# Kernel tuning notes

Measured on AMD Instinct MI355X. Metric: run time of the kernel, lower is better.

Reference implementation:

```python
import jax, jax.numpy as jnp
import numpy as np

B, T, L = 256, 512, 64


def setup_inputs() -> dict:
    key = jax.random.key(0)
    k1, k2, k3 = jax.random.split(key, 3)
    labels = jax.random.randint(k1, (B, T), 0, L)
    y_true = jax.nn.one_hot(labels, L, dtype=jnp.float32)  # [B,T,L] one-hot gold path
    y_pred = jax.random.normal(k2, (B, T, L), dtype=jnp.float32)  # emission scores
    # glorot_uniform init for trans [L,L]
    limit = np.sqrt(6.0 / (L + L)).astype(np.float32)
    trans = jax.random.uniform(k3, (L, L), dtype=jnp.float32, minval=-limit, maxval=limit)
    return {"y_true": y_true, "y_pred": y_pred, "trans": trans}


def reference(y_true, y_pred, trans):
    # ignore_last_label=False -> mask is None, all labels used.
    # Forward-algorithm log-partition via scan over time.
    init = y_pred[:, 0]  # [B,L]

    def step(state, emit_t):
        # state: [B,L] log-alpha; emit_t: [B,L]
        new = jax.nn.logsumexp(state[:, :, None] + trans[None, :, :], axis=1) + emit_t
        return new, None

    emits = jnp.swapaxes(y_pred[:, 1:], 0, 1)  # [T-1,B,L]
    last, _ = jax.lax.scan(step, init, emits)
    log_norm = jax.nn.logsumexp(last, axis=1, keepdims=True)  # [B,1]

    # path_score: per-label emission score + transition score along gold path
    point_score = jnp.sum(y_pred * y_true, axis=(1, 2))[:, None]  # [B,1]
    trans_score = jnp.einsum('bti,btj,ij->b', y_true[:, :-1], y_true[:, 1:], trans)[:, None]
    return -(point_score + trans_score - log_norm)  # [B,1] loss per example
```

## Files before the change

### kernel.cpp

```cpp
#include <hip/hip_runtime.h>
#include <hip/hip_bf16.h>
#include <cstdint>
#include <cstddef>


constexpr int Bc = 256, Tc = 512, Lc = 64;
#define LOG64F 4.1588830833596715f
#define WS_SCAL_OFF (16u << 20)

typedef __attribute__((ext_vector_type(8))) short v8s;
typedef __attribute__((ext_vector_type(4))) float v4f;
typedef __attribute__((ext_vector_type(4))) unsigned int v4u;
typedef __attribute__((ext_vector_type(2))) unsigned int v2u;

__device__ __forceinline__ float lane_bcast(float v, int lane) {
    return __uint_as_float(__builtin_amdgcn_readlane(__float_as_uint(v), lane));
}
__device__ __forceinline__ int lane_bcast_i(int v, int lane) {
    return __builtin_amdgcn_readlane(v, lane);
}
__device__ __forceinline__ unsigned pk2(float x, float y) {
    __hip_bfloat162 h = __float22bfloat162_rn(make_float2(x, y));
    unsigned r; __builtin_memcpy(&r, &h, 4); return r;
}
__device__ __forceinline__ v8s as_v8s(v4u u) {
    v8s r; __builtin_memcpy(&r, &u, 16); return r;
}

__global__ __launch_bounds__(256, 2) void crf_pass1(
    const float* __restrict__ y_true,
    const float* __restrict__ y_pred,
    const float* __restrict__ trans,
    unsigned short* __restrict__ wsm,
    float* __restrict__ wss)
{
    const int tid = threadIdx.x, lane = tid & 63, wv = tid >> 6;
    const int w = blockIdx.x * 4 + wv;
    const int batch = w >> 3, chunk = w & 7;
    const int q = lane >> 4, m16 = lane & 15;
    const int rsub = q, csub = m16;

    __shared__ float strans[Lc * Lc];
    __shared__ alignas(16) float fbuf[4][2][4][Lc];

    {
        const v4f* t4 = (const v4f*)trans;
        #pragma unroll
        for (int k = 0; k < 4; ++k) {
            v4f v = t4[k * 256 + tid];
            *(v4f*)&strans[(k * 256 + tid) * 4] = v;
        }
    }
    __syncthreads();

    v8s Af[4][2];
    #pragma unroll
    for (int I = 0; I < 4; ++I) {
        #pragma unroll
        for (int K = 0; K < 2; ++K) {
            float e[8];
            #pragma unroll
            for (int jj = 0; jj < 8; ++jj) {
                const int sig = (jj & 3) + 4 * q + 16 * (jj >> 2) + 32 * K;
                e[jj] = __expf(strans[sig * Lc + 16 * I + m16]);
            }
            v4u u;
            u.x = pk2(e[0], e[1]); u.y = pk2(e[2], e[3]);
            u.z = pk2(e[4], e[5]); u.w = pk2(e[6], e[7]);
            Af[I][K] = as_v8s(u);
        }
    }

    const float* yp = y_pred + (size_t)batch * Tc * Lc;
    const float* yt = y_true + (size_t)batch * Tc * Lc;
    const v4f* yp4 = (const v4f*)yp;
    const v4f* yt4 = (const v4f*)yt;

    const int base = chunk * 64;
    int lbl_carry;
    {
        const float bt = yt[base * Lc + lane];
        lbl_carry = (int)__builtin_ctzll(__ballot(bt > 0.5f));
    }
    float psum = 0.0f, tsum = 0.0f, c = 0.0f;

    auto ld4 = [&](const v4f* p, int baseRow) -> v4f {
        int r = baseRow + rsub; r = (r < Tc - 1) ? r : (Tc - 1);
        return p[r * 16 + csub];
    };

    const int r0 = base + 1;
    v4f cyp = ld4(yp4, r0),     cyt = ld4(yt4, r0);
    v4f nyp = ld4(yp4, r0 + 4), nyt = ld4(yt4, r0 + 4);
    v4f myp = ld4(yp4, r0 + 8), myt = ld4(yt4, r0 + 8);

    {
        const float k0 = lane_bcast(cyp.x, 0)  + LOG64F;
        const float k1 = lane_bcast(cyp.x, 16) + LOG64F;
        const float k2 = lane_bcast(cyp.x, 32) + LOG64F;
        const float k3 = lane_bcast(cyp.x, 48) + LOG64F;
        c += ((k0 + k1) + (k2 + k3));
        const float kk = (rsub & 1) ? ((rsub & 2) ? k3 : k1)
                                    : ((rsub & 2) ? k2 : k0);
        v4f f;
        f.x = __expf(cyp.x - kk); f.y = __expf(cyp.y - kk);
        f.z = __expf(cyp.z - kk); f.w = __expf(cyp.w - kk);
        *(v4f*)&fbuf[wv][0][rsub][4 * csub] = f;
    }

    v8s Bfr[2][4];
    #pragma unroll
    for (int K = 0; K < 2; ++K) {
        #pragma unroll
        for (int J = 0; J < 4; ++J) {
            v8s bb;
            #pragma unroll
            for (int jj = 0; jj < 8; ++jj) {
                const bool one = (csub == 4 * q + (jj & 3)) && (J == (jj >> 2) + 2 * K);
                bb[jj] = one ? (short)0x3F80 : (short)0;
            }
            Bfr[K][J] = bb;
        }
    }

    const v4f z4 = {0.f, 0.f, 0.f, 0.f};
    v4f P[4][4];
    #pragma unroll
    for (int I = 0; I < 4; ++I) {
        #pragma unroll
        for (int J = 0; J < 4; ++J) P[I][J] = z4;
    }
    int par = 0;

    auto mstep = [&](int s) {
        v4f F[4];
        #pragma unroll
        for (int I = 0; I < 4; ++I)
            F[I] = *(const v4f*)&fbuf[wv][par][s][16 * I + 4 * q];
        #pragma unroll
        for (int I = 0; I < 4; ++I) {
            #pragma unroll
            for (int J = 0; J < 4; ++J) {
                v4f a = __builtin_amdgcn_mfma_f32_16x16x32_bf16(Af[I][0], Bfr[0][J], z4, 0, 0, 0);
                a = __builtin_amdgcn_mfma_f32_16x16x32_bf16(Af[I][1], Bfr[1][J], a, 0, 0, 0);
                P[I][J] = a * F[I];
            }
        }
        #pragma unroll
        for (int K = 0; K < 2; ++K) {
            #pragma unroll
            for (int J = 0; J < 4; ++J) {
                v4u u;
                u.x = pk2(P[2 * K][J].x,     P[2 * K][J].y);
                u.y = pk2(P[2 * K][J].z,     P[2 * K][J].w);
                u.z = pk2(P[2 * K + 1][J].x, P[2 * K + 1][J].y);
                u.w = pk2(P[2 * K + 1][J].z, P[2 * K + 1][J].w);
                Bfr[K][J] = as_v8s(u);
            }
        }
    };

    auto scores4 = [&]() {
        psum = fmaf(cyp.x, cyt.x, psum); psum = fmaf(cyp.y, cyt.y, psum);
        psum = fmaf(cyp.z, cyt.z, psum); psum = fmaf(cyp.w, cyt.w, psum);
        const float has = fmaxf(fmaxf(cyt.x, cyt.y), fmaxf(cyt.z, cyt.w));
        int lidx = 0;
        lidx = (cyt.y > 0.5f) ? 1 : lidx;
        lidx = (cyt.z > 0.5f) ? 2 : lidx;
        lidx = (cyt.w > 0.5f) ? 3 : lidx;
        const unsigned long long m = __ballot(has > 0.5f);
        const int ln0 = (int)__builtin_ctz((unsigned)(m & 0xFFFFull));
        const int ln1 = (int)__builtin_ctz((unsigned)((m >> 16) & 0xFFFFull));
        const int ln2 = (int)__builtin_ctz((unsigned)((m >> 32) & 0xFFFFull));
        const int ln3 = (int)__builtin_ctz((unsigned)(m >> 48));
        const int lbl0 = 4 * ln0 + lane_bcast_i(lidx, ln0);
        const int lbl1 = 4 * ln1 + lane_bcast_i(lidx, 16 + ln1);
        const int lbl2 = 4 * ln2 + lane_bcast_i(lidx, 32 + ln2);
        const int lbl3 = 4 * ln3 + lane_bcast_i(lidx, 48 + ln3);
        const int lpA = (rsub & 2) ? lbl1 : lbl_carry;
        const int lpB = (rsub & 2) ? lbl2 : lbl0;
        const int lp  = (rsub & 1) ? lpB : lpA;
        lbl_carry = lbl3;
        const v4f tr = *(const v4f*)&strans[lp * Lc + 4 * csub];
        tsum = fmaf(cyt.x, tr.x, tsum); tsum = fmaf(cyt.y, tr.y, tsum);
        tsum = fmaf(cyt.z, tr.z, tsum); tsum = fmaf(cyt.w, tr.w, tsum);
    };

    #pragma unroll 1
    for (int bi = 0; bi < 15; ++bi) {
        const int rb = r0 + 4 * bi;
        const v4f lyp = ld4(yp4, rb + 12), lyt = ld4(yt4, rb + 12);
        scores4();
        mstep(0); mstep(1); mstep(2); mstep(3);
        {
            const float sc = lane_bcast(P[0][0].x, 0);
            const float inv_s = 1.0f / sc;
            c += __logf(sc);
            const float k0 = lane_bcast(nyp.x, 0)  + LOG64F;
            const float k1 = lane_bcast(nyp.x, 16) + LOG64F;
            const float k2 = lane_bcast(nyp.x, 32) + LOG64F;
            const float k3 = lane_bcast(nyp.x, 48) + LOG64F;
            c += ((k0 + k1) + k2);
            if (rb + 7 <= Tc - 1) c += k3;
            const float kk = (rsub & 1) ? ((rsub & 2) ? k3 : k1)
                                        : ((rsub & 2) ? k2 : k0);
            const float sc0 = (rsub == 0) ? inv_s : 1.0f;
            v4f f;
            f.x = __expf(nyp.x - kk) * sc0; f.y = __expf(nyp.y - kk) * sc0;
            f.z = __expf(nyp.z - kk) * sc0; f.w = __expf(nyp.w - kk) * sc0;
            *(v4f*)&fbuf[wv][par ^ 1][rsub][4 * csub] = f;
        }
        par ^= 1;
        cyp = nyp; cyt = nyt; nyp = myp; nyt = myt; myp = lyp; myt = lyt;
    }

    if (chunk < 7) {
        scores4();
        mstep(0); mstep(1); mstep(2); mstep(3);
    } else {
        {
            float pd = cyp.x * cyt.x;
            pd = fmaf(cyp.y, cyt.y, pd); pd = fmaf(cyp.z, cyt.z, pd); pd = fmaf(cyp.w, cyt.w, pd);
            const float has = fmaxf(fmaxf(cyt.x, cyt.y), fmaxf(cyt.z, cyt.w));
            int lidx = 0;
            lidx = (cyt.y > 0.5f) ? 1 : lidx;
            lidx = (cyt.z > 0.5f) ? 2 : lidx;
            lidx = (cyt.w > 0.5f) ? 3 : lidx;
            const unsigned long long m = __ballot(has > 0.5f);
            const int ln0 = (int)__builtin_ctz((unsigned)(m & 0xFFFFull));
            const int ln1 = (int)__builtin_ctz((unsigned)((m >> 16) & 0xFFFFull));
            const int lbl0 = 4 * ln0 + lane_bcast_i(lidx, ln0);
            const int lbl1 = 4 * ln1 + lane_bcast_i(lidx, 16 + ln1);
            const int lpA = (rsub & 2) ? lbl1 : lbl_carry;
            const int lp  = (rsub & 1) ? lbl0 : lpA;
            const v4f tr = *(const v4f*)&strans[lp * Lc + 4 * csub];
            float td = cyt.x * tr.x;
            td = fmaf(cyt.y, tr.y, td); td = fmaf(cyt.z, tr.z, td); td = fmaf(cyt.w, tr.w, td);
            if (rsub < 3) { psum += pd; tsum += td; }
        }
        mstep(0); mstep(1); mstep(2);
    }

    unsigned short* hout = wsm + (size_t)(batch * 8 + chunk) * 4096;
    #pragma unroll
    for (int I = 0; I < 4; ++I) {
        #pragma unroll
        for (int J = 0; J < 4; ++J) {
            v2u u2;
            u2.x = pk2(P[I][J].x, P[I][J].y);
            u2.y = pk2(P[I][J].z, P[I][J].w);
            *(v2u*)(hout + (16 * J + csub) * 64 + 16 * I + 4 * q) = u2;
        }
    }
    #pragma unroll
    for (int k = 1; k < 64; k <<= 1) psum += __shfl_xor(psum, k);
    #pragma unroll
    for (int k = 1; k < 64; k <<= 1) tsum += __shfl_xor(tsum, k);
    if (lane == 0) {
        float* s = wss + (batch * 8 + chunk) * 4;
        s[0] = c; s[1] = psum; s[2] = tsum;
    }
}

__global__ __launch_bounds__(256, 1) void crf_pass2(
    const float* __restrict__ y_true,
    const float* __restrict__ y_pred,
    const unsigned short* __restrict__ wsm,
    const float* __restrict__ wss,
    float* __restrict__ out)
{
    const int tid = threadIdx.x, lane = tid & 63, wv = tid >> 6;
    const int b = blockIdx.x * 4 + wv;
    const int q = lane >> 4, m16 = lane & 15;

    __shared__ unsigned short hmat[4][4096];
    __shared__ float arow[4][Lc];

    const float* yp = y_pred + (size_t)b * Tc * Lc;
    const float* yt = y_true + (size_t)b * Tc * Lc;
    const float yp0 = yp[lane], yt0 = yt[lane];
    float psum = yp0 * yt0, tsum = 0.0f;
    float c = lane_bcast(yp0, 0);
    arow[wv][lane] = __expf(yp0 - c);

    v8s Bfr[2];
    #pragma unroll
    for (int cc = 0; cc < 2; ++cc) {
        const v4f lo = *(const v4f*)&arow[wv][32 * cc + 4 * q];
        const v4f hi = *(const v4f*)&arow[wv][32 * cc + 16 + 4 * q];
        v4u u;
        u.x = pk2(lo.x, lo.y); u.y = pk2(lo.z, lo.w);
        u.z = pk2(hi.x, hi.y); u.w = pk2(hi.z, hi.w);
        Bfr[cc] = as_v8s(u);
    }

    const v4f z4 = {0.f, 0.f, 0.f, 0.f};
    v4f P0 = z4, P1 = z4, P2 = z4, P3 = z4;

    #pragma unroll 1
    for (int kk = 0; kk < 8; ++kk) {
        const v4u* src = (const v4u*)(wsm + (size_t)(b * 8 + kk) * 4096);
        #pragma unroll
        for (int i = 0; i < 8; ++i)
            *(v4u*)&hmat[wv][(i * 64 + lane) * 8] = src[i * 64 + lane];

        v8s Afr[4][2];
        #pragma unroll
        for (int I = 0; I < 4; ++I) {
            #pragma unroll
            for (int K = 0; K < 2; ++K) {
                v4u u;
                #pragma unroll
                for (int p = 0; p < 4; ++p) {
                    const int jj = 2 * p;
                    const int sig = (jj & 3) + 4 * q + 16 * (jj >> 2) + 32 * K;
                    const unsigned h0 = hmat[wv][sig * 64 + 16 * I + m16];
                    const unsigned h1 = hmat[wv][(sig + 1) * 64 + 16 * I + m16];
                    u[p] = h0 | (h1 << 16);
                }
                Afr[I][K] = as_v8s(u);
            }
        }

        v4f a0 = __builtin_amdgcn_mfma_f32_16x16x32_bf16(Afr[0][0], Bfr[0], z4, 0, 0, 0);
        v4f a1 = __builtin_amdgcn_mfma_f32_16x16x32_bf16(Afr[1][0], Bfr[0], z4, 0, 0, 0);
        v4f a2 = __builtin_amdgcn_mfma_f32_16x16x32_bf16(Afr[2][0], Bfr[0], z4, 0, 0, 0);
        v4f a3 = __builtin_amdgcn_mfma_f32_16x16x32_bf16(Afr[3][0], Bfr[0], z4, 0, 0, 0);
        a0 = __builtin_amdgcn_mfma_f32_16x16x32_bf16(Afr[0][1], Bfr[1], a0, 0, 0, 0);
        a1 = __builtin_amdgcn_mfma_f32_16x16x32_bf16(Afr[1][1], Bfr[1], a1, 0, 0, 0);
        a2 = __builtin_amdgcn_mfma_f32_16x16x32_bf16(Afr[2][1], Bfr[1], a2, 0, 0, 0);
        a3 = __builtin_amdgcn_mfma_f32_16x16x32_bf16(Afr[3][1], Bfr[1], a3, 0, 0, 0);

        const float sc = lane_bcast(a0.x, 0);
        const float inv = 1.0f / sc;
        c += __logf(sc);
        P0 = a0 * inv; P1 = a1 * inv; P2 = a2 * inv; P3 = a3 * inv;
        {
            v4u u;
            u.x = pk2(P0.x, P0.y); u.y = pk2(P0.z, P0.w);
            u.z = pk2(P1.x, P1.y); u.w = pk2(P1.z, P1.w);
            Bfr[0] = as_v8s(u);
        }
        {
            v4u u;
            u.x = pk2(P2.x, P2.y); u.y = pk2(P2.z, P2.w);
            u.z = pk2(P3.x, P3.y); u.w = pk2(P3.z, P3.w);
            Bfr[1] = as_v8s(u);
        }
    }

    float ftot = (((P0.x + P0.y) + (P0.z + P0.w)) + ((P1.x + P1.y) + (P1.z + P1.w)))
               + (((P2.x + P2.y) + (P2.z + P2.w)) + ((P3.x + P3.y) + (P3.z + P3.w)));
    ftot += __shfl_xor(ftot, 16);
    ftot += __shfl_xor(ftot, 32);

    #pragma unroll
    for (int k = 1; k < 64; k <<= 1) psum += __shfl_xor(psum, k);
    #pragma unroll
    for (int k = 1; k < 64; k <<= 1) tsum += __shfl_xor(tsum, k);

    if (lane == 0) {
        float cs = c, ps = psum, ts = tsum;
        #pragma unroll
        for (int kk = 0; kk < 8; ++kk) {
            const float* s = wss + (b * 8 + kk) * 4;
            cs += s[0]; ps += s[1]; ts += s[2];
        }
        out[b] = -(ps + ts - (cs + __logf(ftot)));
    }
}

extern "C" void kernel_launch(void* const* d_in, const int* in_sizes, int n_in,
                              void* d_out, int out_size, void* d_ws, size_t ws_size,
                              hipStream_t stream) {
    const float* y_true = (const float*)d_in[0];
    const float* y_pred = (const float*)d_in[1];
    const float* trans  = (const float*)d_in[2];
    float* outp = (float*)d_out;
    unsigned short* wsm = (unsigned short*)d_ws;
    float* wss = (float*)((char*)d_ws + WS_SCAL_OFF);
    crf_pass1<<<dim3(512), dim3(256), 0, stream>>>(y_true, y_pred, trans, wsm, wss);
    crf_pass2<<<dim3(64), dim3(256), 0, stream>>>(y_true, y_pred, wsm, wss, outp);
}
```

Measured before the change: 172.1 us.

## Split CRF chunk columns across two waves and prefetch pre-laid-out blobs in pass2

Pass1 now gives each time chunk to two waves, each computing half the output columns of the transition-product matrix. The exp(trans) A fragments are built once per block in LDS and shared, instead of held in registers by every wave. The grid doubles, occupancy is raised, and the per-block rescaling of the running product is dropped. The chunk result is written in an MFMA-ready layout through LDS, so pass2 runs one wave per batch, loads A fragments straight from global memory with double-buffered prefetch, and skips the LDS shuffle. The risks are range drift in the bf16 products from the removed renormalization, and extra LDS traffic per step.

```diff
diff --git a/kernel.cpp b/kernel.cpp
--- a/kernel.cpp
+++ b/kernel.cpp
@@ -11,7 +11,6 @@
 typedef __attribute__((ext_vector_type(8))) short v8s;
 typedef __attribute__((ext_vector_type(4))) float v4f;
 typedef __attribute__((ext_vector_type(4))) unsigned int v4u;
-typedef __attribute__((ext_vector_type(2))) unsigned int v2u;
 
 __device__ __forceinline__ float lane_bcast(float v, int lane) {
     return __uint_as_float(__builtin_amdgcn_readlane(__float_as_uint(v), lane));
@@ -26,8 +25,12 @@
 __device__ __forceinline__ v8s as_v8s(v4u u) {
     v8s r; __builtin_memcpy(&r, &u, 16); return r;
 }
-
-__global__ __launch_bounds__(256, 2) void crf_pass1(
+__device__ __forceinline__ unsigned short bf16b(float x) {
+    __hip_bfloat16 h = __float2bfloat16(x);
+    unsigned short r; __builtin_memcpy(&r, &h, 2); return r;
+}
+
+__global__ __launch_bounds__(256, 4) void crf_pass1(
     const float* __restrict__ y_true,
     const float* __restrict__ y_pred,
     const float* __restrict__ trans,
@@ -36,12 +39,14 @@
 {
     const int tid = threadIdx.x, lane = tid & 63, wv = tid >> 6;
     const int w = blockIdx.x * 4 + wv;
-    const int batch = w >> 3, chunk = w & 7;
+    const int batch = w >> 4, chunk = (w >> 1) & 7, h = w & 1;
     const int q = lane >> 4, m16 = lane & 15;
     const int rsub = q, csub = m16;
 
-    __shared__ float strans[Lc * Lc];
+    __shared__ alignas(16) unsigned char smem_raw[16384];
+    float* strans = (float*)smem_raw;
     __shared__ alignas(16) float fbuf[4][2][4][Lc];
+    __shared__ alignas(16) unsigned short Ablob[8 * 64 * 8];
 
     {
         const v4f* t4 = (const v4f*)trans;
@@ -53,23 +58,20 @@
     }
     __syncthreads();
 
-    v8s Af[4][2];
-    #pragma unroll
-    for (int I = 0; I < 4; ++I) {
-        #pragma unroll
-        for (int K = 0; K < 2; ++K) {
-            float e[8];
-            #pragma unroll
-            for (int jj = 0; jj < 8; ++jj) {
-                const int sig = (jj & 3) + 4 * q + 16 * (jj >> 2) + 32 * K;
-                e[jj] = __expf(strans[sig * Lc + 16 * I + m16]);
-            }
-            v4u u;
-            u.x = pk2(e[0], e[1]); u.y = pk2(e[2], e[3]);
-            u.z = pk2(e[4], e[5]); u.w = pk2(e[6], e[7]);
-            Af[I][K] = as_v8s(u);
-        }
-    }
+    #pragma unroll
+    for (int K = 0; K < 2; ++K) {
+        float e[8];
+        #pragma unroll
+        for (int jj = 0; jj < 8; ++jj) {
+            const int sig = (jj & 3) + 4 * q + 16 * (jj >> 2) + 32 * K;
+            e[jj] = __expf(strans[sig * Lc + 16 * wv + m16]);
+        }
+        v4u u;
+        u.x = pk2(e[0], e[1]); u.y = pk2(e[2], e[3]);
+        u.z = pk2(e[4], e[5]); u.w = pk2(e[6], e[7]);
+        *(v4u*)&Ablob[((wv * 2 + K) * 64 + lane) * 8] = u;
+    }
+    __syncthreads();
 
     const float* yp = y_pred + (size_t)batch * Tc * Lc;
     const float* yt = y_true + (size_t)batch * Tc * Lc;
@@ -77,22 +79,23 @@
     const v4f* yt4 = (const v4f*)yt;
 
     const int base = chunk * 64;
-    int lbl_carry;
-    {
+    const int r0 = base + 1;
+    float psum = 0.0f, tsum = 0.0f, c = 0.0f;
+    int lbl_carry = 0;
+    if (h == 0) {
         const float bt = yt[base * Lc + lane];
         lbl_carry = (int)__builtin_ctzll(__ballot(bt > 0.5f));
     }
-    float psum = 0.0f, tsum = 0.0f, c = 0.0f;
 
     auto ld4 = [&](const v4f* p, int baseRow) -> v4f {
         int r = baseRow + rsub; r = (r < Tc - 1) ? r : (Tc - 1);
         return p[r * 16 + csub];
     };
 
-    const int r0 = base + 1;
-    v4f cyp = ld4(yp4, r0),     cyt = ld4(yt4, r0);
-    v4f nyp = ld4(yp4, r0 + 4), nyt = ld4(yt4, r0 + 4);
-    v4f myp = ld4(yp4, r0 + 8), myt = ld4(yt4, r0 + 8);
+    const v4f z4 = {0.f, 0.f, 0.f, 0.f};
+    v4f cyp = ld4(yp4, r0), nyp = ld4(yp4, r0 + 4);
+    v4f cyt = z4, nyt = z4;
+    if (h == 0) { cyt = ld4(yt4, r0); nyt = ld4(yt4, r0 + 4); }
 
     {
         const float k0 = lane_bcast(cyp.x, 0)  + LOG64F;
@@ -108,54 +111,50 @@
         *(v4f*)&fbuf[wv][0][rsub][4 * csub] = f;
     }
 
-    v8s Bfr[2][4];
-    #pragma unroll
-    for (int K = 0; K < 2; ++K) {
-        #pragma unroll
-        for (int J = 0; J < 4; ++J) {
+    v8s Bfr[2][2];
+    #pragma unroll
+    for (int Kc = 0; Kc < 2; ++Kc) {
+        #pragma unroll
+        for (int Jl = 0; Jl < 2; ++Jl) {
             v8s bb;
             #pragma unroll
             for (int jj = 0; jj < 8; ++jj) {
-                const bool one = (csub == 4 * q + (jj & 3)) && (J == (jj >> 2) + 2 * K);
+                const bool one = (m16 == 4 * q + (jj & 3)) &&
+                                 (2 * h + Jl == (jj >> 2) + 2 * Kc);
                 bb[jj] = one ? (short)0x3F80 : (short)0;
             }
-            Bfr[K][J] = bb;
-        }
-    }
-
-    const v4f z4 = {0.f, 0.f, 0.f, 0.f};
-    v4f P[4][4];
-    #pragma unroll
-    for (int I = 0; I < 4; ++I) {
-        #pragma unroll
-        for (int J = 0; J < 4; ++J) P[I][J] = z4;
-    }
+            Bfr[Kc][Jl] = bb;
+        }
+    }
+
+    v4f P[4][2];
+    #pragma unroll
+    for (int I = 0; I < 4; ++I) { P[I][0] = z4; P[I][1] = z4; }
     int par = 0;
 
     auto mstep = [&](int s) {
-        v4f F[4];
-        #pragma unroll
-        for (int I = 0; I < 4; ++I)
-            F[I] = *(const v4f*)&fbuf[wv][par][s][16 * I + 4 * q];
         #pragma unroll
         for (int I = 0; I < 4; ++I) {
-            #pragma unroll
-            for (int J = 0; J < 4; ++J) {
-                v4f a = __builtin_amdgcn_mfma_f32_16x16x32_bf16(Af[I][0], Bfr[0][J], z4, 0, 0, 0);
-                a = __builtin_amdgcn_mfma_f32_16x16x32_bf16(Af[I][1], Bfr[1][J], a, 0, 0, 0);
-                P[I][J] = a * F[I];
+            const v4f F = *(const v4f*)&fbuf[wv][par][s][16 * I + 4 * q];
+            const v8s A0 = as_v8s(*(const v4u*)&Ablob[((I * 2 + 0) * 64 + lane) * 8]);
+            const v8s A1 = as_v8s(*(const v4u*)&Ablob[((I * 2 + 1) * 64 + lane) * 8]);
+            #pragma unroll
+            for (int Jl = 0; Jl < 2; ++Jl) {
+                v4f a = __builtin_amdgcn_mfma_f32_16x16x32_bf16(A0, Bfr[0][Jl], z4, 0, 0, 0);
+                a = __builtin_amdgcn_mfma_f32_16x16x32_bf16(A1, Bfr[1][Jl], a, 0, 0, 0);
+                P[I][Jl] = a * F;
             }
         }
         #pragma unroll
-        for (int K = 0; K < 2; ++K) {
-            #pragma unroll
-            for (int J = 0; J < 4; ++J) {
+        for (int Kc = 0; Kc < 2; ++Kc) {
+            #pragma unroll
+            for (int Jl = 0; Jl < 2; ++Jl) {
                 v4u u;
-                u.x = pk2(P[2 * K][J].x,     P[2 * K][J].y);
-                u.y = pk2(P[2 * K][J].z,     P[2 * K][J].w);
-                u.z = pk2(P[2 * K + 1][J].x, P[2 * K + 1][J].y);
-                u.w = pk2(P[2 * K + 1][J].z, P[2 * K + 1][J].w);
-                Bfr[K][J] = as_v8s(u);
+                u.x = pk2(P[2 * Kc][Jl].x,     P[2 * Kc][Jl].y);
+                u.y = pk2(P[2 * Kc][Jl].z,     P[2 * Kc][Jl].w);
+                u.z = pk2(P[2 * Kc + 1][Jl].x, P[2 * Kc + 1][Jl].y);
+                u.w = pk2(P[2 * Kc + 1][Jl].z, P[2 * Kc + 1][Jl].w);
+                Bfr[Kc][Jl] = as_v8s(u);
             }
         }
     };
@@ -189,13 +188,14 @@
     #pragma unroll 1
     for (int bi = 0; bi < 15; ++bi) {
         const int rb = r0 + 4 * bi;
-        const v4f lyp = ld4(yp4, rb + 12), lyt = ld4(yt4, rb + 12);
-        scores4();
+        const v4f lyp = ld4(yp4, rb + 8);
+        v4f lyt = z4;
+        if (h == 0) lyt = ld4(yt4, rb + 8);
+
+        if (h == 0) scores4();
         mstep(0); mstep(1); mstep(2); mstep(3);
+
         {
-            const float sc = lane_bcast(P[0][0].x, 0);
-            const float inv_s = 1.0f / sc;
-            c += __logf(sc);
             const float k0 = lane_bcast(nyp.x, 0)  + LOG64F;
             const float k1 = lane_bcast(nyp.x, 16) + LOG64F;
             const float k2 = lane_bcast(nyp.x, 32) + LOG64F;
@@ -204,21 +204,21 @@
             if (rb + 7 <= Tc - 1) c += k3;
             const float kk = (rsub & 1) ? ((rsub & 2) ? k3 : k1)
                                         : ((rsub & 2) ? k2 : k0);
-            const float sc0 = (rsub == 0) ? inv_s : 1.0f;
             v4f f;
-            f.x = __expf(nyp.x - kk) * sc0; f.y = __expf(nyp.y - kk) * sc0;
-            f.z = __expf(nyp.z - kk) * sc0; f.w = __expf(nyp.w - kk) * sc0;
+            f.x = __expf(nyp.x - kk); f.y = __expf(nyp.y - kk);
+            f.z = __expf(nyp.z - kk); f.w = __expf(nyp.w - kk);
             *(v4f*)&fbuf[wv][par ^ 1][rsub][4 * csub] = f;
         }
         par ^= 1;
-        cyp = nyp; cyt = nyt; nyp = myp; nyt = myt; myp = lyp; myt = lyt;
+        cyp = nyp; nyp = lyp;
+        if (h == 0) { cyt = nyt; nyt = lyt; }
     }
 
     if (chunk < 7) {
-        scores4();
+        if (h == 0) scores4();
         mstep(0); mstep(1); mstep(2); mstep(3);
     } else {
-        {
+        if (h == 0) {
             float pd = cyp.x * cyt.x;
             pd = fmaf(cyp.y, cyt.y, pd); pd = fmaf(cyp.z, cyt.z, pd); pd = fmaf(cyp.w, cyt.w, pd);
             const float has = fmaxf(fmaxf(cyt.x, cyt.y), fmaxf(cyt.z, cyt.w));
@@ -241,53 +241,69 @@
         mstep(0); mstep(1); mstep(2);
     }
 
-    unsigned short* hout = wsm + (size_t)(batch * 8 + chunk) * 4096;
+    __syncthreads();
+    unsigned short* myblob = ((unsigned short*)smem_raw) + wv * 2048;
     #pragma unroll
     for (int I = 0; I < 4; ++I) {
         #pragma unroll
-        for (int J = 0; J < 4; ++J) {
-            v2u u2;
-            u2.x = pk2(P[I][J].x, P[I][J].y);
-            u2.y = pk2(P[I][J].z, P[I][J].w);
-            *(v2u*)(hout + (16 * J + csub) * 64 + 16 * I + 4 * q) = u2;
-        }
-    }
-    #pragma unroll
-    for (int k = 1; k < 64; k <<= 1) psum += __shfl_xor(psum, k);
-    #pragma unroll
-    for (int k = 1; k < 64; k <<= 1) tsum += __shfl_xor(tsum, k);
-    if (lane == 0) {
-        float* s = wss + (batch * 8 + chunk) * 4;
-        s[0] = c; s[1] = psum; s[2] = tsum;
-    }
-}
-
-__global__ __launch_bounds__(256, 1) void crf_pass2(
+        for (int Jl = 0; Jl < 2; ++Jl) {
+            float v[4] = {P[I][Jl].x, P[I][Jl].y, P[I][Jl].z, P[I][Jl].w};
+            #pragma unroll
+            for (int r = 0; r < 4; ++r) {
+                const int li = I * 512 + (16 * (m16 >> 2) + 4 * q + r) * 8
+                             + 4 * Jl + (m16 & 3);
+                myblob[li] = bf16b(v[r]);
+            }
+        }
+    }
+    {
+        const int I = lane >> 4;
+        const unsigned short* src = myblob + lane * 32;
+        unsigned short* dst = wsm + (size_t)(batch * 8 + chunk) * 4096
+                            + I * 1024 + h * 512 + (lane & 15) * 32;
+        #pragma unroll
+        for (int t = 0; t < 4; ++t)
+            *(v4u*)(dst + t * 8) = *(const v4u*)(src + t * 8);
+    }
+
+    if (h == 0) {
+        #pragma unroll
+        for (int k = 1; k < 64; k <<= 1) psum += __shfl_xor(psum, k);
+        #pragma unroll
+        for (int k = 1; k < 64; k <<= 1) tsum += __shfl_xor(tsum, k);
+        if (lane == 0) {
+            float* s = wss + (batch * 8 + chunk) * 4;
+            s[0] = c; s[1] = psum; s[2] = tsum;
+        }
+    }
+}
+
+__global__ __launch_bounds__(64, 1) void crf_pass2(
     const float* __restrict__ y_true,
     const float* __restrict__ y_pred,
     const unsigned short* __restrict__ wsm,
     const float* __restrict__ wss,
     float* __restrict__ out)
 {
-    const int tid = threadIdx.x, lane = tid & 63, wv = tid >> 6;
-    const int b = blockIdx.x * 4 + wv;
-    const int q = lane >> 4, m16 = lane & 15;
-
-    __shared__ unsigned short hmat[4][4096];
-    __shared__ float arow[4][Lc];
+    const int lane = threadIdx.x;
+    const int b = blockIdx.x;
+    const int q = lane >> 4;
+
+    __shared__ float arow[Lc];
 
     const float* yp = y_pred + (size_t)b * Tc * Lc;
     const float* yt = y_true + (size_t)b * Tc * Lc;
     const float yp0 = yp[lane], yt0 = yt[lane];
     float psum = yp0 * yt0, tsum = 0.0f;
     float c = lane_bcast(yp0, 0);
-    arow[wv][lane] = __expf(yp0 - c);
+    arow[lane] = __expf(yp0 - c);
+    (void)yt0;
 
     v8s Bfr[2];
     #pragma unroll
     for (int cc = 0; cc < 2; ++cc) {
-        const v4f lo = *(const v4f*)&arow[wv][32 * cc + 4 * q];
-        const v4f hi = *(const v4f*)&arow[wv][32 * cc + 16 + 4 * q];
+        const v4f lo = *(const v4f*)&arow[32 * cc + 4 * q];
+        const v4f hi = *(const v4f*)&arow[32 * cc + 16 + 4 * q];
         v4u u;
         u.x = pk2(lo.x, lo.y); u.y = pk2(lo.z, lo.w);
         u.z = pk2(hi.x, hi.y); u.w = pk2(hi.z, hi.w);
@@ -297,39 +313,29 @@
     const v4f z4 = {0.f, 0.f, 0.f, 0.f};
     v4f P0 = z4, P1 = z4, P2 = z4, P3 = z4;
 
-    #pragma unroll 1
+    v4u Abuf[2][8];
+    {
+        const v4u* g0 = (const v4u*)(wsm + (size_t)(b * 8) * 4096);
+        #pragma unroll
+        for (int s = 0; s < 8; ++s) Abuf[0][s] = g0[s * 64 + lane];
+    }
+
+    #pragma unroll
     for (int kk = 0; kk < 8; ++kk) {
-        const v4u* src = (const v4u*)(wsm + (size_t)(b * 8 + kk) * 4096);
-        #pragma unroll
-        for (int i = 0; i < 8; ++i)
-            *(v4u*)&hmat[wv][(i * 64 + lane) * 8] = src[i * 64 + lane];
-
-        v8s Afr[4][2];
-        #pragma unroll
-        for (int I = 0; I < 4; ++I) {
-            #pragma unroll
-            for (int K = 0; K < 2; ++K) {
-                v4u u;
-                #pragma unroll
-                for (int p = 0; p < 4; ++p) {
-                    const int jj = 2 * p;
-                    const int sig = (jj & 3) + 4 * q + 16 * (jj >> 2) + 32 * K;
-                    const unsigned h0 = hmat[wv][sig * 64 + 16 * I + m16];
-                    const unsigned h1 = hmat[wv][(sig + 1) * 64 + 16 * I + m16];
-                    u[p] = h0 | (h1 << 16);
-                }
-                Afr[I][K] = as_v8s(u);
-            }
-        }
-
-        v4f a0 = __builtin_amdgcn_mfma_f32_16x16x32_bf16(Afr[0][0], Bfr[0], z4, 0, 0, 0);
-        v4f a1 = __builtin_amdgcn_mfma_f32_16x16x32_bf16(Afr[1][0], Bfr[0], z4, 0, 0, 0);
-        v4f a2 = __builtin_amdgcn_mfma_f32_16x16x32_bf16(Afr[2][0], Bfr[0], z4, 0, 0, 0);
-        v4f a3 = __builtin_amdgcn_mfma_f32_16x16x32_bf16(Afr[3][0], Bfr[0], z4, 0, 0, 0);
-        a0 = __builtin_amdgcn_mfma_f32_16x16x32_bf16(Afr[0][1], Bfr[1], a0, 0, 0, 0);
-        a1 = __builtin_amdgcn_mfma_f32_16x16x32_bf16(Afr[1][1], Bfr[1], a1, 0, 0, 0);
-        a2 = __builtin_amdgcn_mfma_f32_16x16x32_bf16(Afr[2][1], Bfr[1], a2, 0, 0, 0);
-        a3 = __builtin_amdgcn_mfma_f32_16x16x32_bf16(Afr[3][1], Bfr[1], a3, 0, 0, 0);
+        const int cur = kk & 1, nxt = cur ^ 1;
+        if (kk < 7) {
+            const v4u* g1 = (const v4u*)(wsm + (size_t)(b * 8 + kk + 1) * 4096);
+            #pragma unroll
+            for (int s = 0; s < 8; ++s) Abuf[nxt][s] = g1[s * 64 + lane];
+        }
+        v4f a0 = __builtin_amdgcn_mfma_f32_16x16x32_bf16(as_v8s(Abuf[cur][0]), Bfr[0], z4, 0, 0, 0);
+        v4f a1 = __builtin_amdgcn_mfma_f32_16x16x32_bf16(as_v8s(Abuf[cur][2]), Bfr[0], z4, 0, 0, 0);
+        v4f a2 = __builtin_amdgcn_mfma_f32_16x16x32_bf16(as_v8s(Abuf[cur][4]), Bfr[0], z4, 0, 0, 0);
+        v4f a3 = __builtin_amdgcn_mfma_f32_16x16x32_bf16(as_v8s(Abuf[cur][6]), Bfr[0], z4, 0, 0, 0);
+        a0 = __builtin_amdgcn_mfma_f32_16x16x32_bf16(as_v8s(Abuf[cur][1]), Bfr[1], a0, 0, 0, 0);
+        a1 = __builtin_amdgcn_mfma_f32_16x16x32_bf16(as_v8s(Abuf[cur][3]), Bfr[1], a1, 0, 0, 0);
+        a2 = __builtin_amdgcn_mfma_f32_16x16x32_bf16(as_v8s(Abuf[cur][5]), Bfr[1], a2, 0, 0, 0);
+        a3 = __builtin_amdgcn_mfma_f32_16x16x32_bf16(as_v8s(Abuf[cur][7]), Bfr[1], a3, 0, 0, 0);
 
         const float sc = lane_bcast(a0.x, 0);
         const float inv = 1.0f / sc;
@@ -356,8 +362,6 @@
 
     #pragma unroll
     for (int k = 1; k < 64; k <<= 1) psum += __shfl_xor(psum, k);
-    #pragma unroll
-    for (int k = 1; k < 64; k <<= 1) tsum += __shfl_xor(tsum, k);
 
     if (lane == 0) {
         float cs = c, ps = psum, ts = tsum;
@@ -379,6 +383,6 @@
     float* outp = (float*)d_out;
     unsigned short* wsm = (unsigned short*)d_ws;
     float* wss = (float*)((char*)d_ws + WS_SCAL_OFF);
-    crf_pass1<<<dim3(512), dim3(256), 0, stream>>>(y_true, y_pred, trans, wsm, wss);
-    crf_pass2<<<dim3(64), dim3(256), 0, stream>>>(y_true, y_pred, wsm, wss, outp);
-}
+    crf_pass1<<<dim3(1024), dim3(256), 0, stream>>>(y_true, y_pred, trans, wsm, wss);
+    crf_pass2<<<dim3(256), dim3(64), 0, stream>>>(y_true, y_pred, wsm, wss, outp);
+}
```

After: 166.3 us. 3.3% less time.
